# Kernel tuning notes

Measured on AMD Instinct MI355X. Metric: run time of the kernel, lower is better.

The kernel has to match this reference:

```python
import jax, jax.numpy as jnp
import numpy as np

N_NODES = 100000
N_HE = 25000
N_CONN = 400000
D = 256
L = 2
MEAN_EPS = 1e-8   # matches torch code's hyperedge-size epsilon
LN_EPS = 1e-5     # torch LayerNorm default
LRELU_SLOPE = 0.2


def setup_inputs() -> dict:
    key = jax.random.key(0)
    ks = jax.random.split(key, 6)
    s = 1.0 / np.sqrt(D).astype(np.float32)
    return {
        "x": jax.random.normal(ks[0], (N_NODES, D), jnp.float32),
        "node_W": jax.random.normal(ks[1], (L, D, D), jnp.float32) * s,
        "node_b": jnp.zeros((L, D), jnp.float32),
        "he_W": jax.random.normal(ks[2], (L, D, D), jnp.float32) * s,
        "he_b": jnp.zeros((L, D), jnp.float32),
        "ln_g": jnp.ones((L, D), jnp.float32),
        "ln_b": jnp.zeros((L, D), jnp.float32),
        "hyperedge_weight": jax.random.uniform(ks[3], (N_HE,), jnp.float32) + 0.5,
        "node_idx": jax.random.randint(ks[4], (N_CONN,), 0, N_NODES, jnp.int64),
        "he_idx": jax.random.randint(ks[5], (N_CONN,), 0, N_HE, jnp.int64),
    }


def _hg_conv(x, Wn, bn, We, be, g, b, w, node_idx, he_idx, n_he):
    # x: [N, D] node features
    xt = x @ Wn + bn                                   # node_transform
    ones = jnp.ones((node_idx.shape[0],), xt.dtype)
    # nodes -> hyperedges (scatter-mean with +eps as in torch code)
    he_sum = jax.ops.segment_sum(xt[node_idx], he_idx, num_segments=n_he)
    he_cnt = jax.ops.segment_sum(ones, he_idx, num_segments=n_he)
    he = he_sum / (he_cnt[:, None] + MEAN_EPS)
    he = (he @ We + be) * w[:, None]                   # hyperedge_transform + weight
    # hyperedges -> nodes (gather then scatter_mean; zero for isolated nodes)
    n_sum = jax.ops.segment_sum(he[he_idx], node_idx, num_segments=x.shape[0])
    n_cnt = jax.ops.segment_sum(ones, node_idx, num_segments=x.shape[0])
    agg = jnp.where(n_cnt[:, None] > 0, n_sum / jnp.maximum(n_cnt, 1.0)[:, None], 0.0)
    # residual + layernorm + leaky relu (dropout is identity at eval)
    h = agg + xt
    mu = jnp.mean(h, axis=-1, keepdims=True)
    var = jnp.var(h, axis=-1, keepdims=True)
    h = (h - mu) * jax.lax.rsqrt(var + LN_EPS) * g + b
    return jax.nn.leaky_relu(h, LRELU_SLOPE)


def reference(x, node_W, node_b, he_W, he_b, ln_g, ln_b, hyperedge_weight, node_idx, he_idx):
    n_he = hyperedge_weight.shape[0]
    n_layers = node_W.shape[0]
    for i in range(n_layers):
        res = x
        x = _hg_conv(x, node_W[i], node_b[i], he_W[i], he_b[i],
                     ln_g[i], ln_b[i], hyperedge_weight, node_idx, he_idx, n_he)
        if i > 0:
            x = x + res
    return x
```

## Files before the change

### kernel.cpp

```cpp
#include <hip/hip_runtime.h>

#define D 256
#define N_NODES 100000
#define N_HE 25000
#define N_CONN 400000

constexpr float MEAN_EPS = 1e-8f;
constexpr float LN_EPS   = 1e-5f;
constexpr float SLOPE    = 0.2f;

typedef __attribute__((ext_vector_type(8))) short short8;
typedef __attribute__((ext_vector_type(4))) float f32x4;
typedef __attribute__((ext_vector_type(16))) float f32x16;
typedef __attribute__((ext_vector_type(4))) unsigned short ushort4v;

static __device__ __forceinline__ unsigned short f2bf(float f) {
  unsigned int u = __builtin_bit_cast(unsigned int, f);
  u = (u + 0x7FFFu + ((u >> 16) & 1u)) >> 16;
  return (unsigned short)u;
}
static __device__ __forceinline__ float bf2f(unsigned short u) {
  return __builtin_bit_cast(float, (unsigned int)u << 16);
}

__global__ __launch_bounds__(256) void hist_kernel(
    const int* __restrict__ node_idx, const int* __restrict__ he_idx,
    int* __restrict__ he_deg, int* __restrict__ n_deg) {
  int c = blockIdx.x * 256 + threadIdx.x;
  if (c < N_CONN) {
    atomicAdd(&he_deg[he_idx[c]], 1);
    atomicAdd(&n_deg[node_idx[c]], 1);
  }
}

__global__ __launch_bounds__(256) void alloc_kernel(
    const int* __restrict__ he_deg, const int* __restrict__ n_deg,
    int* __restrict__ totals,
    int* __restrict__ he_start, int* __restrict__ he_cur,
    int* __restrict__ n_start, int* __restrict__ n_cur) {
  int i = blockIdx.x * 256 + threadIdx.x;
  if (i < N_HE) {
    int s = atomicAdd(&totals[0], he_deg[i]);
    he_start[i] = s;
    he_cur[i] = s;
  }
  if (i < N_NODES) {
    int s = atomicAdd(&totals[1], n_deg[i]);
    n_start[i] = s;
    n_cur[i] = s;
  }
}

__global__ __launch_bounds__(256) void fill_kernel(
    const int* __restrict__ node_idx, const int* __restrict__ he_idx,
    int* __restrict__ he_cur, int* __restrict__ n_cur,
    int* __restrict__ he_list, int* __restrict__ n_list) {
  int c = blockIdx.x * 256 + threadIdx.x;
  if (c < N_CONN) {
    int n = node_idx[c];
    int e = he_idx[c];
    int p = atomicAdd(&he_cur[e], 1);
    he_list[p] = n;
    int q = atomicAdd(&n_cur[n], 1);
    n_list[q] = e;
  }
}

__global__ __launch_bounds__(256) void convert_w(
    const float* __restrict__ W, unsigned short* __restrict__ Wt) {
  int m = blockIdx.x >> 4;
  int tile = blockIdx.x & 15;
  int k0 = (tile >> 2) * 64, n0 = (tile & 3) * 64;
  const float* Win = W + (size_t)m * 65536;
  unsigned short* Wout = Wt + (size_t)m * 65536;
  __shared__ unsigned short T[64][65];
  int t = threadIdx.x;
  int r = t >> 6, c = t & 63;
  #pragma unroll 4
  for (int i = 0; i < 16; ++i) {
    int kr = i * 4 + r;
    T[kr][c] = f2bf(Win[(size_t)(k0 + kr) * 256 + n0 + c]);
  }
  __syncthreads();
  #pragma unroll 4
  for (int i = 0; i < 16; ++i) {
    int nr = i * 4 + r;
    Wout[(size_t)(n0 + nr) * 256 + k0 + c] = T[c][nr];
  }
}

template <int A_F32, int O_F32>
__global__ __launch_bounds__(256, 2) void gemm32(
    const void* __restrict__ Ain, const unsigned short* __restrict__ Wt,
    const float* __restrict__ bias, const float* __restrict__ hw,
    void* __restrict__ outv, int M, int ntiles) {
  __shared__ unsigned short As[64 * 256];
  const int t = threadIdx.x;
  const int wave = t >> 6, lane = t & 63;
  const int l31 = lane & 31, lhi = lane >> 5;
  const int colbase = wave * 64;

  f32x4 B[2][16];
  #pragma unroll
  for (int ct = 0; ct < 2; ++ct) {
    const unsigned short* bp =
        Wt + (size_t)(colbase + ct * 32 + l31) * 256 + lhi * 8;
    #pragma unroll
    for (int kc = 0; kc < 16; ++kc)
      B[ct][kc] = *(const f32x4*)(bp + kc * 16);
  }
  #pragma unroll
  for (int ct = 0; ct < 2; ++ct)
    #pragma unroll
    for (int kc = 0; kc < 16; ++kc)
      asm volatile("" : "+v"(B[ct][kc]));

  float biasv[2];
  #pragma unroll
  for (int ct = 0; ct < 2; ++ct) biasv[ct] = bias[colbase + ct * 32 + l31];

  for (int tile = blockIdx.x; tile < ntiles; tile += gridDim.x) {
    const int row0 = tile * 64;

    if (A_F32) {
      const float* A = (const float*)Ain;
      #pragma unroll 4
      for (int i = 0; i < 16; ++i) {
        int row = i * 4 + (t >> 6);
        int col4 = t & 63;
        int r = row0 + row;
        float4 v = (r < M) ? ((const float4*)(A + (size_t)r * D))[col4]
                           : make_float4(0.f, 0.f, 0.f, 0.f);
        ushort4v o;
        o[0] = f2bf(v.x); o[1] = f2bf(v.y); o[2] = f2bf(v.z); o[3] = f2bf(v.w);
        unsigned int byte = (unsigned)(row * 512 + col4 * 8) ^ (unsigned)((row & 7) << 4);
        *(ushort4v*)((char*)As + byte) = o;
      }
    } else {
      const unsigned short* A = (const unsigned short*)Ain;
      #pragma unroll 4
      for (int i = 0; i < 8; ++i) {
        int row = i * 8 + (t >> 5);
        int e = t & 31;
        int r = row0 + row;
        short8 v = {};
        if (r < M) v = *(const short8*)(A + (size_t)r * D + e * 8);
        unsigned int byte = (unsigned)(row * 512 + e * 16) ^ (unsigned)((row & 7) << 4);
        *(short8*)((char*)As + byte) = v;
      }
    }
    __syncthreads();

    f32x16 acc00 = (f32x16)0.f, acc01 = (f32x16)0.f;
    f32x16 acc10 = (f32x16)0.f, acc11 = (f32x16)0.f;
    #pragma unroll
    for (int kc = 0; kc < 16; ++kc) {
      int r0 = l31;
      unsigned int ad0 = (unsigned)(r0 * 512 + kc * 32 + lhi * 16) ^ (unsigned)((r0 & 7) << 4);
      short8 a0 = *(const short8*)((const char*)As + ad0);
      int r1 = 32 + l31;
      unsigned int ad1 = (unsigned)(r1 * 512 + kc * 32 + lhi * 16) ^ (unsigned)((r1 & 7) << 4);
      short8 a1 = *(const short8*)((const char*)As + ad1);
      short8 b0 = __builtin_bit_cast(short8, B[0][kc]);
      short8 b1 = __builtin_bit_cast(short8, B[1][kc]);
      acc00 = __builtin_amdgcn_mfma_f32_32x32x16_bf16(a0, b0, acc00, 0, 0, 0);
      acc01 = __builtin_amdgcn_mfma_f32_32x32x16_bf16(a0, b1, acc01, 0, 0, 0);
      acc10 = __builtin_amdgcn_mfma_f32_32x32x16_bf16(a1, b0, acc10, 0, 0, 0);
      acc11 = __builtin_amdgcn_mfma_f32_32x32x16_bf16(a1, b1, acc11, 0, 0, 0);
    }

    #pragma unroll
    for (int rt = 0; rt < 2; ++rt) {
      #pragma unroll
      for (int reg = 0; reg < 16; ++reg) {
        int row = (reg & 3) + 8 * (reg >> 2) + 4 * lhi;
        int grow = row0 + rt * 32 + row;
        if (grow < M) {
          float wv = hw ? hw[grow] : 1.f;
          #pragma unroll
          for (int ct = 0; ct < 2; ++ct) {
            int col = colbase + ct * 32 + l31;
            float v = ((rt == 0) ? (ct == 0 ? acc00[reg] : acc01[reg])
                                 : (ct == 0 ? acc10[reg] : acc11[reg])) + biasv[ct];
            v *= wv;
            if (O_F32) {
              ((float*)outv)[(size_t)grow * D + col] = v;
            } else {
              ((unsigned short*)outv)[(size_t)grow * D + col] = f2bf(v);
            }
          }
        }
      }
    }
    __syncthreads();
  }
}

__global__ __launch_bounds__(256) void gather_he_kernel(
    const unsigned short* __restrict__ xt, const int* __restrict__ he_start,
    const int* __restrict__ he_deg, const int* __restrict__ he_list,
    unsigned short* __restrict__ he_out) {
  int e = blockIdx.x * 4 + (threadIdx.x >> 6);
  if (e >= N_HE) return;
  int lane = threadIdx.x & 63;
  int s = he_start[e];
  int deg = he_deg[e];

  float a0 = 0.f, a1 = 0.f, a2 = 0.f, a3 = 0.f;
  int i = 0;
  for (; i + 4 <= deg; i += 4) {
    int n0 = he_list[s + i + 0];
    int n1 = he_list[s + i + 1];
    int n2 = he_list[s + i + 2];
    int n3 = he_list[s + i + 3];
    ushort4v v0 = ((const ushort4v*)(xt + (size_t)n0 * D))[lane];
    ushort4v v1 = ((const ushort4v*)(xt + (size_t)n1 * D))[lane];
    ushort4v v2 = ((const ushort4v*)(xt + (size_t)n2 * D))[lane];
    ushort4v v3 = ((const ushort4v*)(xt + (size_t)n3 * D))[lane];
    a0 += bf2f(v0[0]) + bf2f(v1[0]) + bf2f(v2[0]) + bf2f(v3[0]);
    a1 += bf2f(v0[1]) + bf2f(v1[1]) + bf2f(v2[1]) + bf2f(v3[1]);
    a2 += bf2f(v0[2]) + bf2f(v1[2]) + bf2f(v2[2]) + bf2f(v3[2]);
    a3 += bf2f(v0[3]) + bf2f(v1[3]) + bf2f(v2[3]) + bf2f(v3[3]);
  }
  for (; i < deg; ++i) {
    int n = he_list[s + i];
    ushort4v v = ((const ushort4v*)(xt + (size_t)n * D))[lane];
    a0 += bf2f(v[0]); a1 += bf2f(v[1]); a2 += bf2f(v[2]); a3 += bf2f(v[3]);
  }
  float inv = 1.0f / ((float)deg + MEAN_EPS);
  ushort4v o;
  o[0] = f2bf(a0 * inv); o[1] = f2bf(a1 * inv);
  o[2] = f2bf(a2 * inv); o[3] = f2bf(a3 * inv);
  ((ushort4v*)(he_out + (size_t)e * D))[lane] = o;
}

__global__ __launch_bounds__(256) void gather_node_finalize(
    const unsigned short* __restrict__ he_feat, const int* __restrict__ n_start,
    const int* __restrict__ n_deg, const int* __restrict__ n_list,
    const unsigned short* __restrict__ xt, const float* __restrict__ g,
    const float* __restrict__ b, const float* __restrict__ res,
    float* __restrict__ out, int add_res) {
  int node = blockIdx.x * 4 + (threadIdx.x >> 6);
  if (node >= N_NODES) return;
  int lane = threadIdx.x & 63;
  int s = n_start[node];
  int deg = n_deg[node];

  float a0 = 0.f, a1 = 0.f, a2 = 0.f, a3 = 0.f;
  int i = 0;
  for (; i + 4 <= deg; i += 4) {
    int e0 = n_list[s + i + 0];
    int e1 = n_list[s + i + 1];
    int e2 = n_list[s + i + 2];
    int e3 = n_list[s + i + 3];
    ushort4v v0 = ((const ushort4v*)(he_feat + (size_t)e0 * D))[lane];
    ushort4v v1 = ((const ushort4v*)(he_feat + (size_t)e1 * D))[lane];
    ushort4v v2 = ((const ushort4v*)(he_feat + (size_t)e2 * D))[lane];
    ushort4v v3 = ((const ushort4v*)(he_feat + (size_t)e3 * D))[lane];
    a0 += bf2f(v0[0]) + bf2f(v1[0]) + bf2f(v2[0]) + bf2f(v3[0]);
    a1 += bf2f(v0[1]) + bf2f(v1[1]) + bf2f(v2[1]) + bf2f(v3[1]);
    a2 += bf2f(v0[2]) + bf2f(v1[2]) + bf2f(v2[2]) + bf2f(v3[2]);
    a3 += bf2f(v0[3]) + bf2f(v1[3]) + bf2f(v2[3]) + bf2f(v3[3]);
  }
  for (; i < deg; ++i) {
    int e = n_list[s + i];
    ushort4v v = ((const ushort4v*)(he_feat + (size_t)e * D))[lane];
    a0 += bf2f(v[0]); a1 += bf2f(v[1]); a2 += bf2f(v[2]); a3 += bf2f(v[3]);
  }
  float inv = deg > 0 ? 1.0f / (float)deg : 0.0f;

  ushort4v xv = ((const ushort4v*)(xt + (size_t)node * D))[lane];
  float h0 = a0 * inv + bf2f(xv[0]);
  float h1 = a1 * inv + bf2f(xv[1]);
  float h2 = a2 * inv + bf2f(xv[2]);
  float h3 = a3 * inv + bf2f(xv[3]);

  float sum = h0 + h1 + h2 + h3;
  float ss  = h0 * h0 + h1 * h1 + h2 * h2 + h3 * h3;
  #pragma unroll
  for (int o = 32; o > 0; o >>= 1) {
    sum += __shfl_xor(sum, o, 64);
    ss  += __shfl_xor(ss, o, 64);
  }
  float mu  = sum * (1.0f / D);
  float var = ss * (1.0f / D) - mu * mu;
  float rstd = rsqrtf(var + LN_EPS);

  float4 gv = ((const float4*)g)[lane];
  float4 bv = ((const float4*)b)[lane];

  float o0 = (h0 - mu) * rstd * gv.x + bv.x;
  float o1 = (h1 - mu) * rstd * gv.y + bv.y;
  float o2 = (h2 - mu) * rstd * gv.z + bv.z;
  float o3 = (h3 - mu) * rstd * gv.w + bv.w;
  o0 = o0 >= 0.f ? o0 : o0 * SLOPE;
  o1 = o1 >= 0.f ? o1 : o1 * SLOPE;
  o2 = o2 >= 0.f ? o2 : o2 * SLOPE;
  o3 = o3 >= 0.f ? o3 : o3 * SLOPE;

  if (add_res) {
    float4 rv = ((const float4*)(res + (size_t)node * D))[lane];
    o0 += rv.x; o1 += rv.y; o2 += rv.z; o3 += rv.w;
  }

  ((float4*)(out + (size_t)node * D))[lane] = make_float4(o0, o1, o2, o3);
}

extern "C" void kernel_launch(void* const* d_in, const int* in_sizes, int n_in,
                              void* d_out, int out_size, void* d_ws, size_t ws_size,
                              hipStream_t stream) {
  const float* x       = (const float*)d_in[0];
  const float* node_W  = (const float*)d_in[1];
  const float* node_b  = (const float*)d_in[2];
  const float* he_W    = (const float*)d_in[3];
  const float* he_b    = (const float*)d_in[4];
  const float* ln_g    = (const float*)d_in[5];
  const float* ln_b    = (const float*)d_in[6];
  const float* hw      = (const float*)d_in[7];
  const int*   node_idx = (const int*)d_in[8];
  const int*   he_idx   = (const int*)d_in[9];
  float* out = (float*)d_out;

  unsigned short* xt     = (unsigned short*)d_ws;
  unsigned short* he_buf = xt + (size_t)N_NODES * D;
  unsigned short* Wt_node = he_buf + (size_t)N_HE * D;
  unsigned short* Wt_he   = Wt_node + 2 * 65536;
  int* he_deg   = (int*)(Wt_he + 2 * 65536);
  int* n_deg    = he_deg + N_HE;
  int* totals   = n_deg + N_NODES;
  int* he_start = totals + 2;
  int* he_cur   = he_start + N_HE;
  int* n_start  = he_cur + N_HE;
  int* n_cur    = n_start + N_NODES;
  int* he_list  = n_cur + N_NODES;
  int* n_list   = he_list + N_CONN;

  convert_w<<<32, 256, 0, stream>>>(node_W, Wt_node);
  convert_w<<<32, 256, 0, stream>>>(he_W, Wt_he);

  hipMemsetAsync(he_deg, 0, (size_t)(N_HE + N_NODES + 2) * sizeof(int), stream);
  hist_kernel<<<(N_CONN + 255) / 256, 256, 0, stream>>>(node_idx, he_idx, he_deg, n_deg);
  alloc_kernel<<<(N_NODES + 255) / 256, 256, 0, stream>>>(
      he_deg, n_deg, totals, he_start, he_cur, n_start, n_cur);
  fill_kernel<<<(N_CONN + 255) / 256, 256, 0, stream>>>(
      node_idx, he_idx, he_cur, n_cur, he_list, n_list);

  const int ntiles_node = (N_NODES + 63) / 64;
  const int ntiles_he   = (N_HE + 63) / 64;
  const int grid_node = 512;
  const int grid_he   = ntiles_he;

  for (int l = 0; l < 2; ++l) {
    const float* xin = (l == 0) ? x : out;
    const float* bn = node_b + (size_t)l * D;
    const float* be = he_b + (size_t)l * D;
    const float* g  = ln_g + (size_t)l * D;
    const float* bb = ln_b + (size_t)l * D;

    gemm32<1, 0><<<grid_node, 256, 0, stream>>>(
        xin, Wt_node + (size_t)l * 65536, bn, nullptr, xt, N_NODES, ntiles_node);
    gather_he_kernel<<<(N_HE + 3) / 4, 256, 0, stream>>>(
        xt, he_start, he_deg, he_list, he_buf);
    gemm32<0, 0><<<grid_he, 256, 0, stream>>>(
        he_buf, Wt_he + (size_t)l * 65536, be, hw, he_buf, N_HE, ntiles_he);
    gather_node_finalize<<<(N_NODES + 3) / 4, 256, 0, stream>>>(
        he_buf, n_start, n_deg, n_list, xt, g, bb, xin, out, l);
  }
}
```

Before: 473.8 us.

## Split GEMM across 8 waves with one tile per block instead of persistent loop

The bf16 MFMA GEMM now launches one block per 64-row tile with 512 threads. Each of 8 waves owns 32 output columns, replacing 4 waves that each held 64 columns and looped over tiles in a persistent grid. This cuts per-wave register use for the weight fragments and accumulators, allowing more resident waves to hide load latency. In exchange, every block reloads its weight slice from global memory and there are many more blocks, with no reuse across tiles.

```diff
diff --git a/kernel.cpp b/kernel.cpp
--- a/kernel.cpp
+++ b/kernel.cpp
@@ -90,109 +90,91 @@
 }
 
 template <int A_F32, int O_F32>
-__global__ __launch_bounds__(256, 2) void gemm32(
+__global__ __launch_bounds__(512, 4) void gemm32(
     const void* __restrict__ Ain, const unsigned short* __restrict__ Wt,
     const float* __restrict__ bias, const float* __restrict__ hw,
-    void* __restrict__ outv, int M, int ntiles) {
+    void* __restrict__ outv, int M) {
   __shared__ unsigned short As[64 * 256];
   const int t = threadIdx.x;
   const int wave = t >> 6, lane = t & 63;
   const int l31 = lane & 31, lhi = lane >> 5;
-  const int colbase = wave * 64;
-
-  f32x4 B[2][16];
-  #pragma unroll
-  for (int ct = 0; ct < 2; ++ct) {
-    const unsigned short* bp =
-        Wt + (size_t)(colbase + ct * 32 + l31) * 256 + lhi * 8;
+  const int colbase = wave * 32;
+  const int row0 = blockIdx.x * 64;
+
+  f32x4 B[16];
+  {
+    const unsigned short* bp = Wt + (size_t)(colbase + l31) * 256 + lhi * 8;
     #pragma unroll
     for (int kc = 0; kc < 16; ++kc)
-      B[ct][kc] = *(const f32x4*)(bp + kc * 16);
+      B[kc] = *(const f32x4*)(bp + kc * 16);
   }
   #pragma unroll
-  for (int ct = 0; ct < 2; ++ct)
+  for (int kc = 0; kc < 16; ++kc)
+    asm volatile("" : "+v"(B[kc]));
+
+  float biasv = bias[colbase + l31];
+
+  if (A_F32) {
+    const float* A = (const float*)Ain;
     #pragma unroll
-    for (int kc = 0; kc < 16; ++kc)
-      asm volatile("" : "+v"(B[ct][kc]));
-
-  float biasv[2];
+    for (int i = 0; i < 8; ++i) {
+      int row = i * 8 + (t >> 6);
+      int col4 = t & 63;
+      int r = row0 + row;
+      float4 v = (r < M) ? ((const float4*)(A + (size_t)r * D))[col4]
+                         : make_float4(0.f, 0.f, 0.f, 0.f);
+      ushort4v o;
+      o[0] = f2bf(v.x); o[1] = f2bf(v.y); o[2] = f2bf(v.z); o[3] = f2bf(v.w);
+      unsigned int byte = (unsigned)(row * 512 + col4 * 8) ^ (unsigned)((row & 7) << 4);
+      *(ushort4v*)((char*)As + byte) = o;
+    }
+  } else {
+    const unsigned short* A = (const unsigned short*)Ain;
+    #pragma unroll
+    for (int i = 0; i < 4; ++i) {
+      int row = i * 16 + (t >> 5);
+      int e = t & 31;
+      int r = row0 + row;
+      short8 v = {};
+      if (r < M) v = *(const short8*)(A + (size_t)r * D + e * 8);
+      unsigned int byte = (unsigned)(row * 512 + e * 16) ^ (unsigned)((row & 7) << 4);
+      *(short8*)((char*)As + byte) = v;
+    }
+  }
+  __syncthreads();
+
+  f32x16 acc0 = (f32x16)0.f, acc1 = (f32x16)0.f;
   #pragma unroll
-  for (int ct = 0; ct < 2; ++ct) biasv[ct] = bias[colbase + ct * 32 + l31];
-
-  for (int tile = blockIdx.x; tile < ntiles; tile += gridDim.x) {
-    const int row0 = tile * 64;
-
-    if (A_F32) {
-      const float* A = (const float*)Ain;
-      #pragma unroll 4
-      for (int i = 0; i < 16; ++i) {
-        int row = i * 4 + (t >> 6);
-        int col4 = t & 63;
-        int r = row0 + row;
-        float4 v = (r < M) ? ((const float4*)(A + (size_t)r * D))[col4]
-                           : make_float4(0.f, 0.f, 0.f, 0.f);
-        ushort4v o;
-        o[0] = f2bf(v.x); o[1] = f2bf(v.y); o[2] = f2bf(v.z); o[3] = f2bf(v.w);
-        unsigned int byte = (unsigned)(row * 512 + col4 * 8) ^ (unsigned)((row & 7) << 4);
-        *(ushort4v*)((char*)As + byte) = o;
-      }
-    } else {
-      const unsigned short* A = (const unsigned short*)Ain;
-      #pragma unroll 4
-      for (int i = 0; i < 8; ++i) {
-        int row = i * 8 + (t >> 5);
-        int e = t & 31;
-        int r = row0 + row;
-        short8 v = {};
-        if (r < M) v = *(const short8*)(A + (size_t)r * D + e * 8);
-        unsigned int byte = (unsigned)(row * 512 + e * 16) ^ (unsigned)((row & 7) << 4);
-        *(short8*)((char*)As + byte) = v;
-      }
-    }
-    __syncthreads();
-
-    f32x16 acc00 = (f32x16)0.f, acc01 = (f32x16)0.f;
-    f32x16 acc10 = (f32x16)0.f, acc11 = (f32x16)0.f;
+  for (int kc = 0; kc < 16; ++kc) {
+    int r0 = l31;
+    unsigned int ad0 = (unsigned)(r0 * 512 + kc * 32 + lhi * 16) ^ (unsigned)((r0 & 7) << 4);
+    short8 a0 = *(const short8*)((const char*)As + ad0);
+    int r1 = 32 + l31;
+    unsigned int ad1 = (unsigned)(r1 * 512 + kc * 32 + lhi * 16) ^ (unsigned)((r1 & 7) << 4);
+    short8 a1 = *(const short8*)((const char*)As + ad1);
+    short8 b = __builtin_bit_cast(short8, B[kc]);
+    acc0 = __builtin_amdgcn_mfma_f32_32x32x16_bf16(a0, b, acc0, 0, 0, 0);
+    acc1 = __builtin_amdgcn_mfma_f32_32x32x16_bf16(a1, b, acc1, 0, 0, 0);
+  }
+
+  const int col = colbase + l31;
+  #pragma unroll
+  for (int rt = 0; rt < 2; ++rt) {
     #pragma unroll
-    for (int kc = 0; kc < 16; ++kc) {
-      int r0 = l31;
-      unsigned int ad0 = (unsigned)(r0 * 512 + kc * 32 + lhi * 16) ^ (unsigned)((r0 & 7) << 4);
-      short8 a0 = *(const short8*)((const char*)As + ad0);
-      int r1 = 32 + l31;
-      unsigned int ad1 = (unsigned)(r1 * 512 + kc * 32 + lhi * 16) ^ (unsigned)((r1 & 7) << 4);
-      short8 a1 = *(const short8*)((const char*)As + ad1);
-      short8 b0 = __builtin_bit_cast(short8, B[0][kc]);
-      short8 b1 = __builtin_bit_cast(short8, B[1][kc]);
-      acc00 = __builtin_amdgcn_mfma_f32_32x32x16_bf16(a0, b0, acc00, 0, 0, 0);
-      acc01 = __builtin_amdgcn_mfma_f32_32x32x16_bf16(a0, b1, acc01, 0, 0, 0);
-      acc10 = __builtin_amdgcn_mfma_f32_32x32x16_bf16(a1, b0, acc10, 0, 0, 0);
-      acc11 = __builtin_amdgcn_mfma_f32_32x32x16_bf16(a1, b1, acc11, 0, 0, 0);
-    }
-
-    #pragma unroll
-    for (int rt = 0; rt < 2; ++rt) {
-      #pragma unroll
-      for (int reg = 0; reg < 16; ++reg) {
-        int row = (reg & 3) + 8 * (reg >> 2) + 4 * lhi;
-        int grow = row0 + rt * 32 + row;
-        if (grow < M) {
-          float wv = hw ? hw[grow] : 1.f;
-          #pragma unroll
-          for (int ct = 0; ct < 2; ++ct) {
-            int col = colbase + ct * 32 + l31;
-            float v = ((rt == 0) ? (ct == 0 ? acc00[reg] : acc01[reg])
-                                 : (ct == 0 ? acc10[reg] : acc11[reg])) + biasv[ct];
-            v *= wv;
-            if (O_F32) {
-              ((float*)outv)[(size_t)grow * D + col] = v;
-            } else {
-              ((unsigned short*)outv)[(size_t)grow * D + col] = f2bf(v);
-            }
-          }
+    for (int reg = 0; reg < 16; ++reg) {
+      int row = (reg & 3) + 8 * (reg >> 2) + 4 * lhi;
+      int grow = row0 + rt * 32 + row;
+      if (grow < M) {
+        float wv = hw ? hw[grow] : 1.f;
+        float v = ((rt == 0) ? acc0[reg] : acc1[reg]) + biasv;
+        v *= wv;
+        if (O_F32) {
+          ((float*)outv)[(size_t)grow * D + col] = v;
+        } else {
+          ((unsigned short*)outv)[(size_t)grow * D + col] = f2bf(v);
         }
       }
     }
-    __syncthreads();
   }
 }
 
@@ -347,8 +329,6 @@
 
   const int ntiles_node = (N_NODES + 63) / 64;
   const int ntiles_he   = (N_HE + 63) / 64;
-  const int grid_node = 512;
-  const int grid_he   = ntiles_he;
 
   for (int l = 0; l < 2; ++l) {
     const float* xin = (l == 0) ? x : out;
@@ -357,12 +337,12 @@
     const float* g  = ln_g + (size_t)l * D;
     const float* bb = ln_b + (size_t)l * D;
 
-    gemm32<1, 0><<<grid_node, 256, 0, stream>>>(
-        xin, Wt_node + (size_t)l * 65536, bn, nullptr, xt, N_NODES, ntiles_node);
+    gemm32<1, 0><<<ntiles_node, 512, 0, stream>>>(
+        xin, Wt_node + (size_t)l * 65536, bn, nullptr, xt, N_NODES);
     gather_he_kernel<<<(N_HE + 3) / 4, 256, 0, stream>>>(
         xt, he_start, he_deg, he_list, he_buf);
-    gemm32<0, 0><<<grid_he, 256, 0, stream>>>(
-        he_buf, Wt_he + (size_t)l * 65536, be, hw, he_buf, N_HE, ntiles_he);
+    gemm32<0, 0><<<ntiles_he, 512, 0, stream>>>(
+        he_buf, Wt_he + (size_t)l * 65536, be, hw, he_buf, N_HE);
     gather_node_finalize<<<(N_NODES + 3) / 4, 256, 0, stream>>>(
         he_buf, n_start, n_deg, n_list, xt, g, bb, xin, out, l);
   }
```

Measured after the change: 464.3 us. 1.02x faster.
